# Optimization experiments

Hardware: AMD Instinct MI355X
Metric: run time of the kernel (lower is better)

## Reference

```python
import jax, jax.numpy as jnp
import numpy as np

S, D, H, F = 4096, 1024, 16, 4096
DH = D // H  # 64
EPS = 1e-6


def _layer_norm(x, scale, bias):
    mu = jnp.mean(x, axis=-1, keepdims=True)
    var = jnp.mean(jnp.square(x - mu), axis=-1, keepdims=True)
    return (x - mu) * jax.lax.rsqrt(var + EPS) * scale + bias


def setup_inputs() -> dict:
    key = jax.random.key(0)
    ks = jax.random.split(key, 12)
    s = 0.02
    return {
        "x": jax.random.normal(ks[0], (S, D), jnp.float32),
        "Wq": jax.random.normal(ks[1], (D, H, DH), jnp.float32) * s,
        "bq": jnp.zeros((H, DH), jnp.float32),
        "Wk": jax.random.normal(ks[2], (D, H, DH), jnp.float32) * s,
        "bk": jnp.zeros((H, DH), jnp.float32),
        "Wv": jax.random.normal(ks[3], (D, H, DH), jnp.float32) * s,
        "bv": jnp.zeros((H, DH), jnp.float32),
        "Wo": jax.random.normal(ks[4], (H, DH, D), jnp.float32) * s,
        "bo": jnp.zeros((D,), jnp.float32),
        "ln1_scale": jnp.ones((D,), jnp.float32),
        "ln1_bias": jnp.zeros((D,), jnp.float32),
        "ln2_scale": jnp.ones((D,), jnp.float32),
        "ln2_bias": jnp.zeros((D,), jnp.float32),
        "W1": jax.random.normal(ks[5], (D, F), jnp.float32) * s,
        "b1": jnp.zeros((F,), jnp.float32),
        "W2": jax.random.normal(ks[6], (F, D), jnp.float32) * s,
        "b2": jnp.zeros((D,), jnp.float32),
    }


def reference(x, Wq, bq, Wk, bk, Wv, bv, Wo, bo,
              ln1_scale, ln1_bias, ln2_scale, ln2_bias,
              W1, b1, W2, b2):
    # --- attention block (pre-LN, no mask, no dropout, no RoPE) ---
    y = _layer_norm(x, ln1_scale, ln1_bias)            # [S, D]
    q = jnp.einsum("sd,dhk->shk", y, Wq) + bq          # [S, H, DH]
    k = jnp.einsum("sd,dhk->shk", y, Wk) + bk
    v = jnp.einsum("sd,dhk->shk", y, Wv) + bv
    scale = jnp.float32(1.0 / np.sqrt(DH))
    scores = jnp.einsum("qhd,khd->hqk", q * scale, k)  # [H, S, S]
    w = jax.nn.softmax(scores, axis=-1)
    ctx = jnp.einsum("hqk,khd->qhd", w, v)             # [S, H, DH]
    attn_out = jnp.einsum("qhd,hdo->qo", ctx, Wo) + bo  # [S, D]
    x = x + attn_out
    # --- FFN block ---
    y = _layer_norm(x, ln2_scale, ln2_bias)
    y = jax.nn.gelu(y @ W1 + b1, approximate=False)
    y = y @ W2 + b2
    return x + y
```

## Files before the change

### kernel.cpp

```cpp
#include <hip/hip_runtime.h>
#include <cstdint>
#include <cstddef>


typedef __attribute__((ext_vector_type(8))) __bf16 bf16x8;
typedef __attribute__((ext_vector_type(4))) float f32x4;
typedef __attribute__((ext_vector_type(2))) float f32x2;
typedef __attribute__((ext_vector_type(16))) float f32x16;
typedef __attribute__((ext_vector_type(4))) unsigned int u32x4;

__device__ inline unsigned short f2bf(float f) {
  unsigned int u = __float_as_uint(f);
  u += 0x7fffu + ((u >> 16) & 1u);
  return (unsigned short)(u >> 16);
}

__device__ inline void gload_lds16(const unsigned short* g, unsigned short* l) {
  __builtin_amdgcn_global_load_lds(
      (const __attribute__((address_space(1))) void*)g,
      (__attribute__((address_space(3))) void*)l, 16, 0, 0);
}

__global__ __launch_bounds__(256) void transpose_cvt(const float* __restrict__ in,
                                                     unsigned short* __restrict__ out,
                                                     int K, int N) {
  __shared__ float t[32][33];
  int nb = blockIdx.x * 32, kb = blockIdx.y * 32;
  int tx = threadIdx.x & 31, ty = threadIdx.x >> 5;
#pragma unroll
  for (int i = 0; i < 32; i += 8)
    t[ty + i][tx] = in[(size_t)(kb + ty + i) * N + nb + tx];
  __syncthreads();
#pragma unroll
  for (int i = 0; i < 32; i += 8)
    out[(size_t)(nb + ty + i) * K + kb + tx] = f2bf(t[tx][ty + i]);
}

__global__ __launch_bounds__(256) void concat3(const float* __restrict__ a,
                                               const float* __restrict__ b,
                                               const float* __restrict__ c,
                                               float* __restrict__ out) {
  int i = blockIdx.x * 256 + threadIdx.x;
  float v = (i < 1024) ? a[i] : (i < 2048 ? b[i - 1024] : c[i - 2048]);
  out[i] = v;
}

__global__ __launch_bounds__(256) void ln_kernel(const float* __restrict__ x,
                                                 const float* __restrict__ gamma,
                                                 const float* __restrict__ beta,
                                                 unsigned short* __restrict__ y) {
  int row = blockIdx.x, tid = threadIdx.x;
  const float4 v = ((const float4*)(x + (size_t)row * 1024))[tid];
  float s = v.x + v.y + v.z + v.w;
#pragma unroll
  for (int off = 1; off < 64; off <<= 1) s += __shfl_xor(s, off);
  __shared__ float red1[4], red2[4];
  int wave = tid >> 6;
  if ((tid & 63) == 0) red1[wave] = s;
  __syncthreads();
  float mu = (red1[0] + red1[1] + red1[2] + red1[3]) * (1.0f / 1024.0f);
  float dx = v.x - mu, dy = v.y - mu, dz = v.z - mu, dw = v.w - mu;
  float s2 = dx * dx + dy * dy + dz * dz + dw * dw;
#pragma unroll
  for (int off = 1; off < 64; off <<= 1) s2 += __shfl_xor(s2, off);
  if ((tid & 63) == 0) red2[wave] = s2;
  __syncthreads();
  float var = (red2[0] + red2[1] + red2[2] + red2[3]) * (1.0f / 1024.0f);
  float inv = rsqrtf(var + 1e-6f);
  int c = tid * 4;
  ushort4 o;
  o.x = f2bf(dx * inv * gamma[c + 0] + beta[c + 0]);
  o.y = f2bf(dy * inv * gamma[c + 1] + beta[c + 1]);
  o.z = f2bf(dz * inv * gamma[c + 2] + beta[c + 2]);
  o.w = f2bf(dw * inv * gamma[c + 3] + beta[c + 3]);
  ((ushort4*)(y + (size_t)row * 1024))[tid] = o;
}

template <int BM, int BN, bool GELU, bool RES, bool OUTBF, bool SCALEQ>
__global__ __launch_bounds__(512, (BM == 256 ? 2 : 4)) void gemm8(
    const unsigned short* __restrict__ A,
    const unsigned short* __restrict__ BT,
    const float* __restrict__ bias,
    const float* __restrict__ res,
    void* __restrict__ out,
    int M, int N, int K) {
  constexpr int MH = BM / 64;
  constexpr int NF = BN / 64;
  constexpr int AU = BM / 64;
  constexpr int BU = BN / 64;
  constexpr int AOFF = BM * 64;
  constexpr int SLOT = (BM + BN) * 64;
  __shared__ unsigned short lds[2 * SLOT];
  (void)M;

  const int nbn = N / BN;
  const int bid = blockIdx.x;
  const int cpx = (int)gridDim.x >> 3;
  const int swzb = (bid & 7) * cpx + (bid >> 3);
  const int bm = swzb / nbn, bn = swzb % nbn;
  const int tid = threadIdx.x;
  const int lane = tid & 63, quad = lane >> 4, l16 = lane & 15;
  const int wm = tid >> 8, wn = (tid >> 6) & 3;

  const int rs = tid >> 3;
  const int xo = ((tid & 7) ^ (rs & 7)) * 8;
  const unsigned short* aSrc = A + (size_t)(bm * BM + rs) * K + xo;
  const unsigned short* bSrc = BT + (size_t)(bn * BN + rs) * K + xo;

  const int sw0 = (quad ^ (l16 & 7)) * 8;
  const int sw1 = ((quad ^ 4) ^ (l16 & 7)) * 8;
  const int aBase = (wm * (BM / 2) + l16) * 64;
  const int bBase = (wn * (BN / 4) + l16) * 64;

  f32x4 acc[2 * MH][NF];
  const f32x4 z4 = {0.f, 0.f, 0.f, 0.f};
#pragma unroll
  for (int i = 0; i < 2 * MH; ++i)
#pragma unroll
    for (int n = 0; n < NF; ++n) acc[i][n] = z4;

  const int NT = K >> 6;
  {
    unsigned short* dA = lds + (size_t)tid * 8;
    unsigned short* dB = lds + AOFF + (size_t)tid * 8;
#pragma unroll
    for (int u = 0; u < AU; ++u) gload_lds16(aSrc + (size_t)u * 64 * K, dA + u * 4096);
#pragma unroll
    for (int u = 0; u < BU; ++u) gload_lds16(bSrc + (size_t)u * 64 * K, dB + u * 4096);
  }

  for (int j = 0; j < NT; ++j) {
    const int s = j & 1;
    asm volatile("s_waitcnt vmcnt(0) lgkmcnt(0)" ::: "memory");
    __builtin_amdgcn_s_barrier();
    __builtin_amdgcn_sched_barrier(0);
    const unsigned short* As = lds + s * SLOT;
    const unsigned short* Bs = As + AOFF;
    unsigned short* stA = lds + (s ^ 1) * SLOT + (size_t)tid * 8;
    unsigned short* stB = stA + AOFF;
    const bool pre = (j + 1 < NT);
    const int kN = (j + 1) << 6;

    bf16x8 af[MH][2], bfr[NF][2];
#pragma unroll
    for (int mm = 0; mm < MH; ++mm) {
      af[mm][0] = *(const bf16x8*)(As + aBase + mm * 1024 + sw0);
      af[mm][1] = *(const bf16x8*)(As + aBase + mm * 1024 + sw1);
    }
#pragma unroll
    for (int nn = 0; nn < 2; ++nn) {
      bfr[nn][0] = *(const bf16x8*)(Bs + bBase + nn * 1024 + sw0);
      bfr[nn][1] = *(const bf16x8*)(Bs + bBase + nn * 1024 + sw1);
    }
    if (pre) {
#pragma unroll
      for (int u = 0; u < AU; ++u)
        gload_lds16(aSrc + (size_t)u * 64 * K + kN, stA + u * 4096);
    }
    __builtin_amdgcn_s_barrier();
    __builtin_amdgcn_s_setprio(1);
#pragma unroll
    for (int mm = 0; mm < MH; ++mm)
#pragma unroll
      for (int nn = 0; nn < 2; ++nn) {
        acc[mm][nn] = __builtin_amdgcn_mfma_f32_16x16x32_bf16(af[mm][0], bfr[nn][0], acc[mm][nn], 0, 0, 0);
        acc[mm][nn] = __builtin_amdgcn_mfma_f32_16x16x32_bf16(af[mm][1], bfr[nn][1], acc[mm][nn], 0, 0, 0);
      }
    __builtin_amdgcn_s_setprio(0);
    if constexpr (NF == 4) {
#pragma unroll
      for (int nn = 2; nn < 4; ++nn) {
        bfr[nn][0] = *(const bf16x8*)(Bs + bBase + nn * 1024 + sw0);
        bfr[nn][1] = *(const bf16x8*)(Bs + bBase + nn * 1024 + sw1);
      }
      if (pre) {
#pragma unroll
        for (int u = 0; u < BU; ++u)
          gload_lds16(bSrc + (size_t)u * 64 * K + kN, stB + u * 4096);
      }
      __builtin_amdgcn_s_barrier();
      __builtin_amdgcn_s_setprio(1);
#pragma unroll
      for (int mm = 0; mm < MH; ++mm)
#pragma unroll
        for (int nn = 2; nn < 4; ++nn) {
          acc[mm][nn] = __builtin_amdgcn_mfma_f32_16x16x32_bf16(af[mm][0], bfr[nn][0], acc[mm][nn], 0, 0, 0);
          acc[mm][nn] = __builtin_amdgcn_mfma_f32_16x16x32_bf16(af[mm][1], bfr[nn][1], acc[mm][nn], 0, 0, 0);
        }
      __builtin_amdgcn_s_setprio(0);
    }
#pragma unroll
    for (int mm = 0; mm < MH; ++mm) {
      af[mm][0] = *(const bf16x8*)(As + aBase + MH * 1024 + mm * 1024 + sw0);
      af[mm][1] = *(const bf16x8*)(As + aBase + MH * 1024 + mm * 1024 + sw1);
    }
    if constexpr (NF == 2) {
      if (pre) {
#pragma unroll
        for (int u = 0; u < BU; ++u)
          gload_lds16(bSrc + (size_t)u * 64 * K + kN, stB + u * 4096);
      }
    }
    __builtin_amdgcn_s_barrier();
    __builtin_amdgcn_s_setprio(1);
#pragma unroll
    for (int mm = 0; mm < MH; ++mm)
#pragma unroll
      for (int nn = 0; nn < 2; ++nn) {
        acc[MH + mm][nn] = __builtin_amdgcn_mfma_f32_16x16x32_bf16(af[mm][0], bfr[nn][0], acc[MH + mm][nn], 0, 0, 0);
        acc[MH + mm][nn] = __builtin_amdgcn_mfma_f32_16x16x32_bf16(af[mm][1], bfr[nn][1], acc[MH + mm][nn], 0, 0, 0);
      }
    __builtin_amdgcn_s_setprio(0);
    if constexpr (NF == 4) {
      __builtin_amdgcn_s_barrier();
      __builtin_amdgcn_s_setprio(1);
#pragma unroll
      for (int mm = 0; mm < MH; ++mm)
#pragma unroll
        for (int nn = 2; nn < 4; ++nn) {
          acc[MH + mm][nn] = __builtin_amdgcn_mfma_f32_16x16x32_bf16(af[mm][0], bfr[nn][0], acc[MH + mm][nn], 0, 0, 0);
          acc[MH + mm][nn] = __builtin_amdgcn_mfma_f32_16x16x32_bf16(af[mm][1], bfr[nn][1], acc[MH + mm][nn], 0, 0, 0);
        }
      __builtin_amdgcn_s_setprio(0);
    }
  }

#pragma unroll
  for (int mi = 0; mi < 2 * MH; ++mi) {
    const int row0 = bm * BM + wm * (BM / 2) + mi * 16 + quad * 4;
#pragma unroll
    for (int ni = 0; ni < NF; ++ni) {
      const int col = bn * BN + wn * (BN / 4) + ni * 16 + l16;
      const float bv = bias[col];
      const float qs = (SCALEQ && col < 1024) ? 0.18033688f : 1.0f;
#pragma unroll
      for (int r = 0; r < 4; ++r) {
        float v = (acc[mi][ni][r] + bv) * qs;
        if (GELU) v = 0.5f * v * (1.0f + erff(v * 0.70710678118654752440f));
        if (RES) v += res[(size_t)(row0 + r) * N + col];
        if (OUTBF)
          ((unsigned short*)out)[(size_t)(row0 + r) * N + col] = f2bf(v);
        else
          ((float*)out)[(size_t)(row0 + r) * N + col] = v;
      }
    }
  }
}

__global__ __launch_bounds__(256) void prep_kv(const unsigned short* __restrict__ qkv,
                                               unsigned short* __restrict__ Kp,
                                               unsigned short* __restrict__ Vp) {
  __shared__ unsigned short Vt[64 * 64];
  int t = blockIdx.x, h = blockIdx.y;
  int tid = threadIdx.x;
  const int r2 = tid >> 3, c0 = (tid & 7) * 8;
  size_t tb = ((size_t)h * 64 + t) * 4096;
  {
    const unsigned short* kp = qkv + (size_t)(t * 64 + r2) * 3072 + 1024 + h * 64 + c0;
    uint4 k0 = *(const uint4*)kp;
    uint4 k1 = *(const uint4*)(kp + (size_t)32 * 3072);
    int c = c0 >> 3;
    *(uint4*)(Kp + tb + c * 512 + r2 * 8) = k0;
    *(uint4*)(Kp + tb + c * 512 + (r2 + 32) * 8) = k1;
  }
  {
    const unsigned short* vp = qkv + (size_t)(t * 64 + 2 * r2) * 3072 + 2048 + h * 64 + c0;
    uint4 v0 = *(const uint4*)vp;
    uint4 v1 = *(const uint4*)(vp + 3072);
    const unsigned short* p0 = (const unsigned short*)&v0;
    const unsigned short* p1 = (const unsigned short*)&v1;
#pragma unroll
    for (int dd = 0; dd < 8; dd++) {
      unsigned int pk = (unsigned int)p0[dd] | ((unsigned int)p1[dd] << 16);
      *(unsigned int*)&Vt[(c0 + dd) * 64 + 2 * r2] = pk;
    }
  }
  __syncthreads();
#pragma unroll
  for (int u0 = 0; u0 < 2; u0++) {
    int u = tid + u0 * 256;
    *(uint4*)(Vp + tb + u * 8) = *(const uint4*)&Vt[(u & 63) * 64 + (u >> 6) * 8];
  }
}

__global__ __launch_bounds__(256, 3) void attn_kernel(const unsigned short* __restrict__ qkv,
                                                      const unsigned short* __restrict__ Kp,
                                                      const unsigned short* __restrict__ Vp,
                                                      unsigned short* __restrict__ ctx) {
  __shared__ float comb[2 * 32 * 64];
  __shared__ float lpart[4 * 32];
  int qt = blockIdx.x, h = blockIdx.y;
  int tid = threadIdx.x;
  int w = tid >> 6, lane = tid & 63;
  int l31 = lane & 31, hi = lane >> 5;
  int qsub = w & 1, kvh = w >> 1;

  bf16x8 qf[4];
  {
    const unsigned short* qp = qkv + (size_t)(qt * 64 + qsub * 32 + l31) * 3072 + h * 64 + hi * 8;
#pragma unroll
    for (int kk = 0; kk < 4; kk++) qf[kk] = *(const bf16x8*)(qp + kk * 16);
  }

  const size_t hb = (size_t)h * 64 * 4096;
  const unsigned short* kB = Kp + hb + hi * 512 + (kvh * 32 + l31) * 8;
  const unsigned short* vB = Vp + hb + (kvh * 4 + hi) * 512 + l31 * 8;

  f32x16 accO0, accO1;
  f32x2 lp2 = {0.f, 0.f};
#pragma unroll
  for (int r = 0; r < 16; r++) { accO0[r] = 0.f; accO1[r] = 0.f; }

  bf16x8 kf[4];
#pragma unroll
  for (int kk = 0; kk < 4; kk++) kf[kk] = *(const bf16x8*)(kB + kk * 1024);

  for (int t = 0; t < 64; t++) {
    const unsigned short* vt = vB + (size_t)t * 4096;
    bf16x8 vA0 = *(const bf16x8*)(vt);
    bf16x8 vA1 = *(const bf16x8*)(vt + 1024);
    bf16x8 vB0 = *(const bf16x8*)(vt + 256);
    bf16x8 vB1 = *(const bf16x8*)(vt + 1024 + 256);

    f32x16 accS;
#pragma unroll
    for (int r = 0; r < 16; r++) accS[r] = 0.f;
#pragma unroll
    for (int kk = 0; kk < 4; kk++)
      accS = __builtin_amdgcn_mfma_f32_32x32x16_bf16(kf[kk], qf[kk], accS, 0, 0, 0);

    if (t < 63) {
      const unsigned short* kt = kB + (size_t)(t + 1) * 4096;
#pragma unroll
      for (int kk = 0; kk < 4; kk++) kf[kk] = *(const bf16x8*)(kt + kk * 1024);
    }

    unsigned int pd[8];
#pragma unroll
    for (int i = 0; i < 8; i++) {
      float a = __builtin_amdgcn_exp2f(accS[2 * i]);
      float b = __builtin_amdgcn_exp2f(accS[2 * i + 1]);
      f32x2 ab = {a, b};
      lp2 += ab;
      pd[i] = __builtin_amdgcn_perm(__float_as_uint(b), __float_as_uint(a), 0x07060302);
    }
    asm("v_permlane32_swap_b32 %0, %1" : "+v"(pd[0]), "+v"(pd[2]));
    asm("v_permlane32_swap_b32 %0, %1" : "+v"(pd[1]), "+v"(pd[3]));
    asm("v_permlane32_swap_b32 %0, %1" : "+v"(pd[4]), "+v"(pd[6]));
    asm("v_permlane32_swap_b32 %0, %1" : "+v"(pd[5]), "+v"(pd[7]));
    u32x4 f0 = {pd[0], pd[1], pd[2], pd[3]};
    u32x4 f1 = {pd[4], pd[5], pd[6], pd[7]};
    bf16x8 pa0 = __builtin_bit_cast(bf16x8, f0);
    bf16x8 pa1 = __builtin_bit_cast(bf16x8, f1);

    accO0 = __builtin_amdgcn_mfma_f32_32x32x16_bf16(pa0, vA0, accO0, 0, 0, 0);
    accO1 = __builtin_amdgcn_mfma_f32_32x32x16_bf16(pa0, vB0, accO1, 0, 0, 0);
    accO0 = __builtin_amdgcn_mfma_f32_32x32x16_bf16(pa1, vA1, accO0, 0, 0, 0);
    accO1 = __builtin_amdgcn_mfma_f32_32x32x16_bf16(pa1, vB1, accO1, 0, 0, 0);
  }

  float lp = lp2.x + lp2.y;
  lp += __shfl_xor(lp, 32);
  if (hi == 0) lpart[(kvh * 2 + qsub) * 32 + l31] = lp;
  if (kvh == 1) {
#pragma unroll
    for (int r = 0; r < 16; r++) {
      int q = (r & 3) + 8 * (r >> 2) + 4 * hi;
      comb[(qsub * 32 + q) * 64 + l31] = accO0[r];
      comb[(qsub * 32 + q) * 64 + 32 + l31] = accO1[r];
    }
  }
  __syncthreads();
  if (kvh == 0) {
#pragma unroll
    for (int r = 0; r < 16; r++) {
      int q = (r & 3) + 8 * (r >> 2) + 4 * hi;
      float l = lpart[qsub * 32 + q] + lpart[(2 + qsub) * 32 + q];
      float inv = 1.0f / l;
      float v0 = (accO0[r] + comb[(qsub * 32 + q) * 64 + l31]) * inv;
      float v1 = (accO1[r] + comb[(qsub * 32 + q) * 64 + 32 + l31]) * inv;
      int row = qt * 64 + qsub * 32 + q;
      size_t o = (size_t)row * 1024 + h * 64;
      ctx[o + l31] = f2bf(v0);
      ctx[o + 32 + l31] = f2bf(v1);
    }
  }
}

extern "C" void kernel_launch(void* const* d_in, const int* in_sizes, int n_in,
                              void* d_out, int out_size, void* d_ws, size_t ws_size,
                              hipStream_t stream) {
  const float* x   = (const float*)d_in[0];
  const float* Wq  = (const float*)d_in[1];
  const float* bq  = (const float*)d_in[2];
  const float* Wk  = (const float*)d_in[3];
  const float* bk  = (const float*)d_in[4];
  const float* Wv  = (const float*)d_in[5];
  const float* bv  = (const float*)d_in[6];
  const float* Wo  = (const float*)d_in[7];
  const float* bo  = (const float*)d_in[8];
  const float* g1  = (const float*)d_in[9];
  const float* be1 = (const float*)d_in[10];
  const float* g2  = (const float*)d_in[11];
  const float* be2 = (const float*)d_in[12];
  const float* W1  = (const float*)d_in[13];
  const float* b1  = (const float*)d_in[14];
  const float* W2  = (const float*)d_in[15];
  const float* b2  = (const float*)d_in[16];
  float* out = (float*)d_out;

  char* p = (char*)d_ws;
  unsigned short* WqkvT = (unsigned short*)p; p += (size_t)3072 * 1024 * 2;
  unsigned short* WoT   = (unsigned short*)p; p += (size_t)1024 * 1024 * 2;
  unsigned short* W1T   = (unsigned short*)p; p += (size_t)4096 * 1024 * 2;
  unsigned short* W2T   = (unsigned short*)p; p += (size_t)1024 * 4096 * 2;
  float*          bqkv  = (float*)p;          p += 16384;
  unsigned short* y1    = (unsigned short*)p; p += (size_t)4096 * 1024 * 2;
  unsigned short* qkvb  = (unsigned short*)p; p += (size_t)4096 * 3072 * 2;
  unsigned short* ctxb  = (unsigned short*)p; p += (size_t)4096 * 1024 * 2;
  float*          x1    = (float*)p;          p += (size_t)4096 * 1024 * 4;
  unsigned short* Kp    = (unsigned short*)p; p += (size_t)16 * 64 * 4096 * 2;
  unsigned short* Vp    = (unsigned short*)p; p += (size_t)16 * 64 * 4096 * 2;
  unsigned short* hbuf  = qkvb;

  dim3 b256(256);
  dim3 b512(512);
  transpose_cvt<<<dim3(32, 32), b256, 0, stream>>>(Wq, WqkvT, 1024, 1024);
  transpose_cvt<<<dim3(32, 32), b256, 0, stream>>>(Wk, WqkvT + (size_t)1024 * 1024, 1024, 1024);
  transpose_cvt<<<dim3(32, 32), b256, 0, stream>>>(Wv, WqkvT + (size_t)2048 * 1024, 1024, 1024);
  transpose_cvt<<<dim3(32, 32), b256, 0, stream>>>(Wo, WoT, 1024, 1024);
  transpose_cvt<<<dim3(128, 32), b256, 0, stream>>>(W1, W1T, 1024, 4096);
  transpose_cvt<<<dim3(32, 128), b256, 0, stream>>>(W2, W2T, 4096, 1024);
  concat3<<<12, b256, 0, stream>>>(bq, bk, bv, bqkv);

  ln_kernel<<<4096, b256, 0, stream>>>(x, g1, be1, y1);
  gemm8<256, 256, false, false, true, true><<<dim3(192), b512, 0, stream>>>(y1, WqkvT, bqkv, nullptr, qkvb, 4096, 3072, 1024);
  prep_kv<<<dim3(64, 16), b256, 0, stream>>>(qkvb, Kp, Vp);
  attn_kernel<<<dim3(64, 16), b256, 0, stream>>>(qkvb, Kp, Vp, ctxb);
  gemm8<128, 128, false, true, false, false><<<dim3(256), b512, 0, stream>>>(ctxb, WoT, bo, x, x1, 4096, 1024, 1024);
  ln_kernel<<<4096, b256, 0, stream>>>(x1, g2, be2, y1);
  gemm8<256, 256, true, false, true, false><<<dim3(256), b512, 0, stream>>>(y1, W1T, b1, nullptr, hbuf, 4096, 4096, 1024);
  gemm8<128, 128, false, true, false, false><<<dim3(256), b512, 0, stream>>>(hbuf, W2T, b2, x1, out, 4096, 1024, 4096);
}
```

Baseline: 390.3 us.

## Add triple-buffered 128x128 GEMM and double-buffer K/V fragments in attention

Adds a new 128x128 GEMM kernel with a three-slot LDS ring that prefetches two K-tiles ahead, using a partial vmcnt wait so loads overlap compute. The Wo and W2 projections now use it. The 256x256 GEMM is specialized to a fixed tile and issues all A/B prefetches in the first phase. The attention loop is unrolled by two with ping-pong K and V register fragments, so V for the next tile is loaded early instead of at the start of each iteration. The cost is more LDS per block and higher register pressure in attention.

```diff
diff --git a/kernel.cpp b/kernel.cpp
--- a/kernel.cpp
+++ b/kernel.cpp
@@ -76,24 +76,19 @@
   ((ushort4*)(y + (size_t)row * 1024))[tid] = o;
 }
 
-template <int BM, int BN, bool GELU, bool RES, bool OUTBF, bool SCALEQ>
-__global__ __launch_bounds__(512, (BM == 256 ? 2 : 4)) void gemm8(
+template <bool GELU, bool RES, bool OUTBF, bool SCALEQ>
+__global__ __launch_bounds__(512, 2) void gemm8(
     const unsigned short* __restrict__ A,
     const unsigned short* __restrict__ BT,
     const float* __restrict__ bias,
     const float* __restrict__ res,
     void* __restrict__ out,
     int M, int N, int K) {
-  constexpr int MH = BM / 64;
-  constexpr int NF = BN / 64;
-  constexpr int AU = BM / 64;
-  constexpr int BU = BN / 64;
-  constexpr int AOFF = BM * 64;
-  constexpr int SLOT = (BM + BN) * 64;
+  constexpr int SLOT = 512 * 64;
   __shared__ unsigned short lds[2 * SLOT];
   (void)M;
 
-  const int nbn = N / BN;
+  const int nbn = N / 256;
   const int bid = blockIdx.x;
   const int cpx = (int)gridDim.x >> 3;
   const int swzb = (bid & 7) * cpx + (bid >> 3);
@@ -104,29 +99,29 @@
 
   const int rs = tid >> 3;
   const int xo = ((tid & 7) ^ (rs & 7)) * 8;
-  const unsigned short* aSrc = A + (size_t)(bm * BM + rs) * K + xo;
-  const unsigned short* bSrc = BT + (size_t)(bn * BN + rs) * K + xo;
+  const unsigned short* aSrc = A + (size_t)(bm * 256 + rs) * K + xo;
+  const unsigned short* bSrc = BT + (size_t)(bn * 256 + rs) * K + xo;
 
   const int sw0 = (quad ^ (l16 & 7)) * 8;
   const int sw1 = ((quad ^ 4) ^ (l16 & 7)) * 8;
-  const int aBase = (wm * (BM / 2) + l16) * 64;
-  const int bBase = (wn * (BN / 4) + l16) * 64;
-
-  f32x4 acc[2 * MH][NF];
+  const int aBase = (wm * 128 + l16) * 64;
+  const int bBase = 16384 + (wn * 64 + l16) * 64;
+
+  f32x4 acc[8][4];
   const f32x4 z4 = {0.f, 0.f, 0.f, 0.f};
 #pragma unroll
-  for (int i = 0; i < 2 * MH; ++i)
-#pragma unroll
-    for (int n = 0; n < NF; ++n) acc[i][n] = z4;
+  for (int i = 0; i < 8; ++i)
+#pragma unroll
+    for (int n = 0; n < 4; ++n) acc[i][n] = z4;
 
   const int NT = K >> 6;
   {
     unsigned short* dA = lds + (size_t)tid * 8;
-    unsigned short* dB = lds + AOFF + (size_t)tid * 8;
-#pragma unroll
-    for (int u = 0; u < AU; ++u) gload_lds16(aSrc + (size_t)u * 64 * K, dA + u * 4096);
-#pragma unroll
-    for (int u = 0; u < BU; ++u) gload_lds16(bSrc + (size_t)u * 64 * K, dB + u * 4096);
+    unsigned short* dB = lds + 16384 + (size_t)tid * 8;
+#pragma unroll
+    for (int u = 0; u < 4; ++u) gload_lds16(aSrc + (size_t)u * 64 * K, dA + u * 4096);
+#pragma unroll
+    for (int u = 0; u < 4; ++u) gload_lds16(bSrc + (size_t)u * 64 * K, dB + u * 4096);
   }
 
   for (int j = 0; j < NT; ++j) {
@@ -134,108 +129,227 @@
     asm volatile("s_waitcnt vmcnt(0) lgkmcnt(0)" ::: "memory");
     __builtin_amdgcn_s_barrier();
     __builtin_amdgcn_sched_barrier(0);
-    const unsigned short* As = lds + s * SLOT;
-    const unsigned short* Bs = As + AOFF;
+    const unsigned short* Ts = lds + s * SLOT;
     unsigned short* stA = lds + (s ^ 1) * SLOT + (size_t)tid * 8;
-    unsigned short* stB = stA + AOFF;
+    unsigned short* stB = stA + 16384;
     const bool pre = (j + 1 < NT);
     const int kN = (j + 1) << 6;
 
-    bf16x8 af[MH][2], bfr[NF][2];
-#pragma unroll
-    for (int mm = 0; mm < MH; ++mm) {
-      af[mm][0] = *(const bf16x8*)(As + aBase + mm * 1024 + sw0);
-      af[mm][1] = *(const bf16x8*)(As + aBase + mm * 1024 + sw1);
+    bf16x8 af[4][2], bfr[4][2];
+#pragma unroll
+    for (int mm = 0; mm < 4; ++mm) {
+      af[mm][0] = *(const bf16x8*)(Ts + aBase + mm * 1024 + sw0);
+      af[mm][1] = *(const bf16x8*)(Ts + aBase + mm * 1024 + sw1);
     }
 #pragma unroll
     for (int nn = 0; nn < 2; ++nn) {
-      bfr[nn][0] = *(const bf16x8*)(Bs + bBase + nn * 1024 + sw0);
-      bfr[nn][1] = *(const bf16x8*)(Bs + bBase + nn * 1024 + sw1);
+      bfr[nn][0] = *(const bf16x8*)(Ts + bBase + nn * 1024 + sw0);
+      bfr[nn][1] = *(const bf16x8*)(Ts + bBase + nn * 1024 + sw1);
     }
     if (pre) {
 #pragma unroll
-      for (int u = 0; u < AU; ++u)
+      for (int u = 0; u < 4; ++u)
         gload_lds16(aSrc + (size_t)u * 64 * K + kN, stA + u * 4096);
+#pragma unroll
+      for (int u = 0; u < 4; ++u)
+        gload_lds16(bSrc + (size_t)u * 64 * K + kN, stB + u * 4096);
     }
     __builtin_amdgcn_s_barrier();
     __builtin_amdgcn_s_setprio(1);
 #pragma unroll
-    for (int mm = 0; mm < MH; ++mm)
+    for (int mm = 0; mm < 4; ++mm)
 #pragma unroll
       for (int nn = 0; nn < 2; ++nn) {
         acc[mm][nn] = __builtin_amdgcn_mfma_f32_16x16x32_bf16(af[mm][0], bfr[nn][0], acc[mm][nn], 0, 0, 0);
         acc[mm][nn] = __builtin_amdgcn_mfma_f32_16x16x32_bf16(af[mm][1], bfr[nn][1], acc[mm][nn], 0, 0, 0);
       }
     __builtin_amdgcn_s_setprio(0);
-    if constexpr (NF == 4) {
+#pragma unroll
+    for (int nn = 2; nn < 4; ++nn) {
+      bfr[nn][0] = *(const bf16x8*)(Ts + bBase + nn * 1024 + sw0);
+      bfr[nn][1] = *(const bf16x8*)(Ts + bBase + nn * 1024 + sw1);
+    }
+    __builtin_amdgcn_s_barrier();
+    __builtin_amdgcn_s_setprio(1);
+#pragma unroll
+    for (int mm = 0; mm < 4; ++mm)
 #pragma unroll
       for (int nn = 2; nn < 4; ++nn) {
-        bfr[nn][0] = *(const bf16x8*)(Bs + bBase + nn * 1024 + sw0);
-        bfr[nn][1] = *(const bf16x8*)(Bs + bBase + nn * 1024 + sw1);
-      }
-      if (pre) {
-#pragma unroll
-        for (int u = 0; u < BU; ++u)
-          gload_lds16(bSrc + (size_t)u * 64 * K + kN, stB + u * 4096);
-      }
-      __builtin_amdgcn_s_barrier();
-      __builtin_amdgcn_s_setprio(1);
-#pragma unroll
-      for (int mm = 0; mm < MH; ++mm)
-#pragma unroll
-        for (int nn = 2; nn < 4; ++nn) {
-          acc[mm][nn] = __builtin_amdgcn_mfma_f32_16x16x32_bf16(af[mm][0], bfr[nn][0], acc[mm][nn], 0, 0, 0);
-          acc[mm][nn] = __builtin_amdgcn_mfma_f32_16x16x32_bf16(af[mm][1], bfr[nn][1], acc[mm][nn], 0, 0, 0);
-        }
-      __builtin_amdgcn_s_setprio(0);
-    }
-#pragma unroll
-    for (int mm = 0; mm < MH; ++mm) {
-      af[mm][0] = *(const bf16x8*)(As + aBase + MH * 1024 + mm * 1024 + sw0);
-      af[mm][1] = *(const bf16x8*)(As + aBase + MH * 1024 + mm * 1024 + sw1);
-    }
-    if constexpr (NF == 2) {
-      if (pre) {
-#pragma unroll
-        for (int u = 0; u < BU; ++u)
-          gload_lds16(bSrc + (size_t)u * 64 * K + kN, stB + u * 4096);
-      }
+        acc[mm][nn] = __builtin_amdgcn_mfma_f32_16x16x32_bf16(af[mm][0], bfr[nn][0], acc[mm][nn], 0, 0, 0);
+        acc[mm][nn] = __builtin_amdgcn_mfma_f32_16x16x32_bf16(af[mm][1], bfr[nn][1], acc[mm][nn], 0, 0, 0);
+      }
+    __builtin_amdgcn_s_setprio(0);
+#pragma unroll
+    for (int mm = 0; mm < 4; ++mm) {
+      af[mm][0] = *(const bf16x8*)(Ts + aBase + 4096 + mm * 1024 + sw0);
+      af[mm][1] = *(const bf16x8*)(Ts + aBase + 4096 + mm * 1024 + sw1);
     }
     __builtin_amdgcn_s_barrier();
     __builtin_amdgcn_s_setprio(1);
 #pragma unroll
-    for (int mm = 0; mm < MH; ++mm)
+    for (int mm = 0; mm < 4; ++mm)
 #pragma unroll
       for (int nn = 0; nn < 2; ++nn) {
-        acc[MH + mm][nn] = __builtin_amdgcn_mfma_f32_16x16x32_bf16(af[mm][0], bfr[nn][0], acc[MH + mm][nn], 0, 0, 0);
-        acc[MH + mm][nn] = __builtin_amdgcn_mfma_f32_16x16x32_bf16(af[mm][1], bfr[nn][1], acc[MH + mm][nn], 0, 0, 0);
+        acc[4 + mm][nn] = __builtin_amdgcn_mfma_f32_16x16x32_bf16(af[mm][0], bfr[nn][0], acc[4 + mm][nn], 0, 0, 0);
+        acc[4 + mm][nn] = __builtin_amdgcn_mfma_f32_16x16x32_bf16(af[mm][1], bfr[nn][1], acc[4 + mm][nn], 0, 0, 0);
       }
     __builtin_amdgcn_s_setprio(0);
-    if constexpr (NF == 4) {
-      __builtin_amdgcn_s_barrier();
-      __builtin_amdgcn_s_setprio(1);
-#pragma unroll
-      for (int mm = 0; mm < MH; ++mm)
-#pragma unroll
-        for (int nn = 2; nn < 4; ++nn) {
-          acc[MH + mm][nn] = __builtin_amdgcn_mfma_f32_16x16x32_bf16(af[mm][0], bfr[nn][0], acc[MH + mm][nn], 0, 0, 0);
-          acc[MH + mm][nn] = __builtin_amdgcn_mfma_f32_16x16x32_bf16(af[mm][1], bfr[nn][1], acc[MH + mm][nn], 0, 0, 0);
-        }
-      __builtin_amdgcn_s_setprio(0);
-    }
-  }
-
-#pragma unroll
-  for (int mi = 0; mi < 2 * MH; ++mi) {
-    const int row0 = bm * BM + wm * (BM / 2) + mi * 16 + quad * 4;
-#pragma unroll
-    for (int ni = 0; ni < NF; ++ni) {
-      const int col = bn * BN + wn * (BN / 4) + ni * 16 + l16;
+    __builtin_amdgcn_s_barrier();
+    __builtin_amdgcn_s_setprio(1);
+#pragma unroll
+    for (int mm = 0; mm < 4; ++mm)
+#pragma unroll
+      for (int nn = 2; nn < 4; ++nn) {
+        acc[4 + mm][nn] = __builtin_amdgcn_mfma_f32_16x16x32_bf16(af[mm][0], bfr[nn][0], acc[4 + mm][nn], 0, 0, 0);
+        acc[4 + mm][nn] = __builtin_amdgcn_mfma_f32_16x16x32_bf16(af[mm][1], bfr[nn][1], acc[4 + mm][nn], 0, 0, 0);
+      }
+    __builtin_amdgcn_s_setprio(0);
+  }
+
+#pragma unroll
+  for (int mi = 0; mi < 8; ++mi) {
+    const int row0 = bm * 256 + wm * 128 + mi * 16 + quad * 4;
+#pragma unroll
+    for (int ni = 0; ni < 4; ++ni) {
+      const int col = bn * 256 + wn * 64 + ni * 16 + l16;
       const float bv = bias[col];
       const float qs = (SCALEQ && col < 1024) ? 0.18033688f : 1.0f;
 #pragma unroll
       for (int r = 0; r < 4; ++r) {
         float v = (acc[mi][ni][r] + bv) * qs;
+        if (GELU) v = 0.5f * v * (1.0f + erff(v * 0.70710678118654752440f));
+        if (RES) v += res[(size_t)(row0 + r) * N + col];
+        if (OUTBF)
+          ((unsigned short*)out)[(size_t)(row0 + r) * N + col] = f2bf(v);
+        else
+          ((float*)out)[(size_t)(row0 + r) * N + col] = v;
+      }
+    }
+  }
+}
+
+template <bool GELU, bool RES, bool OUTBF>
+__global__ __launch_bounds__(512, 2) void gemm3s(
+    const unsigned short* __restrict__ A,
+    const unsigned short* __restrict__ BT,
+    const float* __restrict__ bias,
+    const float* __restrict__ res,
+    void* __restrict__ out,
+    int M, int N, int K) {
+  constexpr int SLOT = 256 * 64;
+  __shared__ unsigned short lds[3 * SLOT];
+  (void)M;
+
+  const int nbn = N / 128;
+  const int bid = blockIdx.x;
+  const int cpx = (int)gridDim.x >> 3;
+  const int swzb = (bid & 7) * cpx + (bid >> 3);
+  const int bm = swzb / nbn, bn = swzb % nbn;
+  const int tid = threadIdx.x;
+  const int lane = tid & 63, quad = lane >> 4, l16 = lane & 15;
+  const int wm = tid >> 8, wn = (tid >> 6) & 3;
+
+  const int rs = tid >> 3;
+  const int xo = ((tid & 7) ^ (rs & 7)) * 8;
+  const unsigned short* aSrc = A + (size_t)(bm * 128 + rs) * K + xo;
+  const unsigned short* bSrc = BT + (size_t)(bn * 128 + rs) * K + xo;
+
+  const int sw0 = (quad ^ (l16 & 7)) * 8;
+  const int sw1 = ((quad ^ 4) ^ (l16 & 7)) * 8;
+  const int aBase = (wm * 64 + l16) * 64;
+  const int bBase = 8192 + (wn * 32 + l16) * 64;
+
+  f32x4 acc[4][2];
+  const f32x4 z4 = {0.f, 0.f, 0.f, 0.f};
+#pragma unroll
+  for (int i = 0; i < 4; ++i)
+#pragma unroll
+    for (int n = 0; n < 2; ++n) acc[i][n] = z4;
+
+  const int NT = K >> 6;
+  {
+    unsigned short* d0 = lds + (size_t)tid * 8;
+    gload_lds16(aSrc, d0);
+    gload_lds16(aSrc + (size_t)64 * K, d0 + 4096);
+    gload_lds16(bSrc, d0 + 8192);
+    gload_lds16(bSrc + (size_t)64 * K, d0 + 8192 + 4096);
+    if (NT > 1) {
+      unsigned short* d1 = lds + SLOT + (size_t)tid * 8;
+      gload_lds16(aSrc + 64, d1);
+      gload_lds16(aSrc + (size_t)64 * K + 64, d1 + 4096);
+      gload_lds16(bSrc + 64, d1 + 8192);
+      gload_lds16(bSrc + (size_t)64 * K + 64, d1 + 8192 + 4096);
+    }
+  }
+
+  int sl = 0;
+  for (int j = 0; j < NT; ++j) {
+    if (j + 1 < NT)
+      asm volatile("s_waitcnt vmcnt(4) lgkmcnt(0)" ::: "memory");
+    else
+      asm volatile("s_waitcnt vmcnt(0) lgkmcnt(0)" ::: "memory");
+    __builtin_amdgcn_s_barrier();
+    __builtin_amdgcn_sched_barrier(0);
+    const unsigned short* Ts = lds + sl * SLOT;
+    const int sl2 = (sl >= 1) ? sl - 1 : 2;
+    unsigned short* st = lds + sl2 * SLOT + (size_t)tid * 8;
+
+    bf16x8 af[2][2], bfr[2][2];
+#pragma unroll
+    for (int mm = 0; mm < 2; ++mm) {
+      af[mm][0] = *(const bf16x8*)(Ts + aBase + mm * 1024 + sw0);
+      af[mm][1] = *(const bf16x8*)(Ts + aBase + mm * 1024 + sw1);
+    }
+#pragma unroll
+    for (int nn = 0; nn < 2; ++nn) {
+      bfr[nn][0] = *(const bf16x8*)(Ts + bBase + nn * 1024 + sw0);
+      bfr[nn][1] = *(const bf16x8*)(Ts + bBase + nn * 1024 + sw1);
+    }
+    if (j + 2 < NT) {
+      const int kN = (j + 2) << 6;
+      gload_lds16(aSrc + kN, st);
+      gload_lds16(aSrc + (size_t)64 * K + kN, st + 4096);
+      gload_lds16(bSrc + kN, st + 8192);
+      gload_lds16(bSrc + (size_t)64 * K + kN, st + 8192 + 4096);
+    }
+    __builtin_amdgcn_s_barrier();
+    __builtin_amdgcn_s_setprio(1);
+#pragma unroll
+    for (int mm = 0; mm < 2; ++mm)
+#pragma unroll
+      for (int nn = 0; nn < 2; ++nn) {
+        acc[mm][nn] = __builtin_amdgcn_mfma_f32_16x16x32_bf16(af[mm][0], bfr[nn][0], acc[mm][nn], 0, 0, 0);
+        acc[mm][nn] = __builtin_amdgcn_mfma_f32_16x16x32_bf16(af[mm][1], bfr[nn][1], acc[mm][nn], 0, 0, 0);
+      }
+    __builtin_amdgcn_s_setprio(0);
+#pragma unroll
+    for (int mm = 0; mm < 2; ++mm) {
+      af[mm][0] = *(const bf16x8*)(Ts + aBase + 2048 + mm * 1024 + sw0);
+      af[mm][1] = *(const bf16x8*)(Ts + aBase + 2048 + mm * 1024 + sw1);
+    }
+    __builtin_amdgcn_s_barrier();
+    __builtin_amdgcn_s_setprio(1);
+#pragma unroll
+    for (int mm = 0; mm < 2; ++mm)
+#pragma unroll
+      for (int nn = 0; nn < 2; ++nn) {
+        acc[2 + mm][nn] = __builtin_amdgcn_mfma_f32_16x16x32_bf16(af[mm][0], bfr[nn][0], acc[2 + mm][nn], 0, 0, 0);
+        acc[2 + mm][nn] = __builtin_amdgcn_mfma_f32_16x16x32_bf16(af[mm][1], bfr[nn][1], acc[2 + mm][nn], 0, 0, 0);
+      }
+    __builtin_amdgcn_s_setprio(0);
+    sl = (sl == 2) ? 0 : sl + 1;
+  }
+
+#pragma unroll
+  for (int mi = 0; mi < 4; ++mi) {
+    const int row0 = bm * 128 + wm * 64 + mi * 16 + quad * 4;
+#pragma unroll
+    for (int ni = 0; ni < 2; ++ni) {
+      const int col = bn * 128 + wn * 32 + ni * 16 + l16;
+      const float bv = bias[col];
+#pragma unroll
+      for (int r = 0; r < 4; ++r) {
+        float v = acc[mi][ni][r] + bv;
         if (GELU) v = 0.5f * v * (1.0f + erff(v * 0.70710678118654752440f));
         if (RES) v += res[(size_t)(row0 + r) * N + col];
         if (OUTBF)
@@ -283,6 +397,47 @@
   }
 }
 
+#define ATTN_STEP(KF, VF, KN, VN, T)                                                  \
+  {                                                                                   \
+    f32x16 accS;                                                                      \
+    _Pragma("unroll")                                                                 \
+    for (int r = 0; r < 16; r++) accS[r] = 0.f;                                       \
+    _Pragma("unroll")                                                                 \
+    for (int kk = 0; kk < 4; kk++)                                                    \
+      accS = __builtin_amdgcn_mfma_f32_32x32x16_bf16(KF[kk], qf[kk], accS, 0, 0, 0);  \
+    if ((T) < 63) {                                                                   \
+      const unsigned short* kt = kB + (size_t)((T) + 1) * 4096;                       \
+      const unsigned short* vt = vB + (size_t)((T) + 1) * 4096;                       \
+      _Pragma("unroll")                                                               \
+      for (int kk = 0; kk < 4; kk++) KN[kk] = *(const bf16x8*)(kt + kk * 1024);       \
+      VN[0] = *(const bf16x8*)(vt);                                                   \
+      VN[1] = *(const bf16x8*)(vt + 1024);                                            \
+      VN[2] = *(const bf16x8*)(vt + 256);                                             \
+      VN[3] = *(const bf16x8*)(vt + 1024 + 256);                                      \
+    }                                                                                 \
+    unsigned int pd[8];                                                               \
+    _Pragma("unroll")                                                                 \
+    for (int i = 0; i < 8; i++) {                                                     \
+      float a = __builtin_amdgcn_exp2f(accS[2 * i]);                                  \
+      float b = __builtin_amdgcn_exp2f(accS[2 * i + 1]);                              \
+      f32x2 ab = {a, b};                                                              \
+      lp2 += ab;                                                                      \
+      pd[i] = __builtin_amdgcn_perm(__float_as_uint(b), __float_as_uint(a), 0x07060302); \
+    }                                                                                 \
+    asm("v_permlane32_swap_b32 %0, %1" : "+v"(pd[0]), "+v"(pd[2]));                   \
+    asm("v_permlane32_swap_b32 %0, %1" : "+v"(pd[1]), "+v"(pd[3]));                   \
+    asm("v_permlane32_swap_b32 %0, %1" : "+v"(pd[4]), "+v"(pd[6]));                   \
+    asm("v_permlane32_swap_b32 %0, %1" : "+v"(pd[5]), "+v"(pd[7]));                   \
+    u32x4 f0 = {pd[0], pd[1], pd[2], pd[3]};                                          \
+    u32x4 f1 = {pd[4], pd[5], pd[6], pd[7]};                                          \
+    bf16x8 pa0 = __builtin_bit_cast(bf16x8, f0);                                      \
+    bf16x8 pa1 = __builtin_bit_cast(bf16x8, f1);                                      \
+    accO0 = __builtin_amdgcn_mfma_f32_32x32x16_bf16(pa0, VF[0], accO0, 0, 0, 0);      \
+    accO1 = __builtin_amdgcn_mfma_f32_32x32x16_bf16(pa0, VF[2], accO1, 0, 0, 0);      \
+    accO0 = __builtin_amdgcn_mfma_f32_32x32x16_bf16(pa1, VF[1], accO0, 0, 0, 0);      \
+    accO1 = __builtin_amdgcn_mfma_f32_32x32x16_bf16(pa1, VF[3], accO1, 0, 0, 0);      \
+  }
+
 __global__ __launch_bounds__(256, 3) void attn_kernel(const unsigned short* __restrict__ qkv,
                                                       const unsigned short* __restrict__ Kp,
                                                       const unsigned short* __restrict__ Vp,
@@ -311,52 +466,17 @@
 #pragma unroll
   for (int r = 0; r < 16; r++) { accO0[r] = 0.f; accO1[r] = 0.f; }
 
-  bf16x8 kf[4];
-#pragma unroll
-  for (int kk = 0; kk < 4; kk++) kf[kk] = *(const bf16x8*)(kB + kk * 1024);
-
-  for (int t = 0; t < 64; t++) {
-    const unsigned short* vt = vB + (size_t)t * 4096;
-    bf16x8 vA0 = *(const bf16x8*)(vt);
-    bf16x8 vA1 = *(const bf16x8*)(vt + 1024);
-    bf16x8 vB0 = *(const bf16x8*)(vt + 256);
-    bf16x8 vB1 = *(const bf16x8*)(vt + 1024 + 256);
-
-    f32x16 accS;
-#pragma unroll
-    for (int r = 0; r < 16; r++) accS[r] = 0.f;
-#pragma unroll
-    for (int kk = 0; kk < 4; kk++)
-      accS = __builtin_amdgcn_mfma_f32_32x32x16_bf16(kf[kk], qf[kk], accS, 0, 0, 0);
-
-    if (t < 63) {
-      const unsigned short* kt = kB + (size_t)(t + 1) * 4096;
-#pragma unroll
-      for (int kk = 0; kk < 4; kk++) kf[kk] = *(const bf16x8*)(kt + kk * 1024);
-    }
-
-    unsigned int pd[8];
-#pragma unroll
-    for (int i = 0; i < 8; i++) {
-      float a = __builtin_amdgcn_exp2f(accS[2 * i]);
-      float b = __builtin_amdgcn_exp2f(accS[2 * i + 1]);
-      f32x2 ab = {a, b};
-      lp2 += ab;
-      pd[i] = __builtin_amdgcn_perm(__float_as_uint(b), __float_as_uint(a), 0x07060302);
-    }
-    asm("v_permlane32_swap_b32 %0, %1" : "+v"(pd[0]), "+v"(pd[2]));
-    asm("v_permlane32_swap_b32 %0, %1" : "+v"(pd[1]), "+v"(pd[3]));
-    asm("v_permlane32_swap_b32 %0, %1" : "+v"(pd[4]), "+v"(pd[6]));
-    asm("v_permlane32_swap_b32 %0, %1" : "+v"(pd[5]), "+v"(pd[7]));
-    u32x4 f0 = {pd[0], pd[1], pd[2], pd[3]};
-    u32x4 f1 = {pd[4], pd[5], pd[6], pd[7]};
-    bf16x8 pa0 = __builtin_bit_cast(bf16x8, f0);
-    bf16x8 pa1 = __builtin_bit_cast(bf16x8, f1);
-
-    accO0 = __builtin_amdgcn_mfma_f32_32x32x16_bf16(pa0, vA0, accO0, 0, 0, 0);
-    accO1 = __builtin_amdgcn_mfma_f32_32x32x16_bf16(pa0, vB0, accO1, 0, 0, 0);
-    accO0 = __builtin_amdgcn_mfma_f32_32x32x16_bf16(pa1, vA1, accO0, 0, 0, 0);
-    accO1 = __builtin_amdgcn_mfma_f32_32x32x16_bf16(pa1, vB1, accO1, 0, 0, 0);
+  bf16x8 kfa[4], vfa[4], kfb[4], vfb[4];
+#pragma unroll
+  for (int kk = 0; kk < 4; kk++) kfa[kk] = *(const bf16x8*)(kB + kk * 1024);
+  vfa[0] = *(const bf16x8*)(vB);
+  vfa[1] = *(const bf16x8*)(vB + 1024);
+  vfa[2] = *(const bf16x8*)(vB + 256);
+  vfa[3] = *(const bf16x8*)(vB + 1024 + 256);
+
+  for (int t = 0; t < 64; t += 2) {
+    ATTN_STEP(kfa, vfa, kfb, vfb, t);
+    ATTN_STEP(kfb, vfb, kfa, vfa, t + 1);
   }
 
   float lp = lp2.x + lp2.y;
@@ -434,11 +554,11 @@
   concat3<<<12, b256, 0, stream>>>(bq, bk, bv, bqkv);
 
   ln_kernel<<<4096, b256, 0, stream>>>(x, g1, be1, y1);
-  gemm8<256, 256, false, false, true, true><<<dim3(192), b512, 0, stream>>>(y1, WqkvT, bqkv, nullptr, qkvb, 4096, 3072, 1024);
+  gemm8<false, false, true, true><<<dim3(192), b512, 0, stream>>>(y1, WqkvT, bqkv, nullptr, qkvb, 4096, 3072, 1024);
   prep_kv<<<dim3(64, 16), b256, 0, stream>>>(qkvb, Kp, Vp);
   attn_kernel<<<dim3(64, 16), b256, 0, stream>>>(qkvb, Kp, Vp, ctxb);
-  gemm8<128, 128, false, true, false, false><<<dim3(256), b512, 0, stream>>>(ctxb, WoT, bo, x, x1, 4096, 1024, 1024);
+  gemm3s<false, true, false><<<dim3(256), b512, 0, stream>>>(ctxb, WoT, bo, x, x1, 4096, 1024, 1024);
   ln_kernel<<<4096, b256, 0, stream>>>(x1, g2, be2, y1);
-  gemm8<256, 256, true, false, true, false><<<dim3(256), b512, 0, stream>>>(y1, W1T, b1, nullptr, hbuf, 4096, 4096, 1024);
-  gemm8<128, 128, false, true, false, false><<<dim3(256), b512, 0, stream>>>(hbuf, W2T, b2, x1, out, 4096, 1024, 4096);
-}
+  gemm8<true, false, true, false><<<dim3(256), b512, 0, stream>>>(y1, W1T, b1, nullptr, hbuf, 4096, 4096, 1024);
+  gemm3s<false, true, false><<<dim3(256), b512, 0, stream>>>(hbuf, W2T, b2, x1, out, 4096, 1024, 4096);
+}
```

Result: no change. 383.6 us (-1.7%).
